# Kernel optimization log

Hardware: AMD Instinct MI355X
Metric: run time of the kernel (lower is better)

The kernel has to match this reference:

```python
import jax, jax.numpy as jnp
import numpy as np

N, E, F, H, C = 100000, 3200000, 128, 256, 47
EPS = 1e-5


def setup_inputs() -> dict:
    key = jax.random.key(0)
    ks = jax.random.split(key, 12)
    x = jax.random.normal(ks[0], (N, F), dtype=jnp.float32)
    edge_index = jax.random.randint(ks[1], (2, E), 0, N, dtype=jnp.int64)
    relations = jax.random.randint(ks[2], (E,), 0, 4, dtype=jnp.int64)
    def lin(k, fan_in, fan_out):
        return jax.random.normal(k, (fan_in, fan_out), dtype=jnp.float32) / np.sqrt(fan_in)
    W0 = lin(ks[3], F, H); b0 = jnp.zeros((H,), jnp.float32)
    W1 = lin(ks[4], H, H); b1 = jnp.zeros((H,), jnp.float32)
    W2 = lin(ks[5], H, C); b2 = jnp.zeros((C,), jnp.float32)
    g0 = jnp.ones((H,), jnp.float32); be0 = jnp.zeros((H,), jnp.float32)
    g1 = jnp.ones((H,), jnp.float32); be1 = jnp.zeros((H,), jnp.float32)
    return {"x": x, "edge_index": edge_index, "relations": relations,
            "W0": W0, "b0": b0, "g0": g0, "be0": be0,
            "W1": W1, "b1": b1, "g1": g1, "be1": be1,
            "W2": W2, "b2": b2}


def _gcn_conv(x, W, b, src, dst, n_nodes):
    # GCNConv: linear transform, add self-loops, symmetric degree normalization,
    # gather-scale-scatter aggregation, bias add.
    h = x @ W  # [N, out]
    self_loop = jnp.arange(n_nodes, dtype=src.dtype)
    s = jnp.concatenate([src, self_loop])
    d = jnp.concatenate([dst, self_loop])
    deg = jax.ops.segment_sum(jnp.ones(d.shape[0], h.dtype), d, num_segments=n_nodes)
    dinv = jnp.where(deg > 0, jax.lax.rsqrt(deg), 0.0)
    coef = dinv[s] * dinv[d]  # [E+N]
    out = jax.ops.segment_sum(h[s] * coef[:, None], d, num_segments=n_nodes)
    return out + b


def _batch_norm(x, gamma, beta):
    mean = jnp.mean(x, axis=0)
    var = jnp.var(x, axis=0)
    return (x - mean) * jax.lax.rsqrt(var + EPS) * gamma + beta


def reference(x, edge_index, relations, W0, b0, g0, be0, W1, b1, g1, be1, W2, b2):
    src, dst = edge_index[0], edge_index[1]
    n = x.shape[0]
    h = _gcn_conv(x, W0, b0, src, dst, n)
    h = jax.nn.relu(_batch_norm(h, g0, be0))  # dropout is identity in eval
    h = _gcn_conv(h, W1, b1, src, dst, n)
    h = jax.nn.relu(_batch_norm(h, g1, be1))
    h = _gcn_conv(h, W2, b2, src, dst, n)
    return jax.nn.log_softmax(h, axis=-1)
```

## Files before the change

### kernel.cpp

```cpp
#include <hip/hip_runtime.h>
#include <hip/hip_fp8.h>
#include <math.h>

#define NN 100000
#define NE 3200000
#define FIN 128
#define HD 256
#define CO 47
#define NBKT 196
#define G 1024
#define CHUNK 3125

typedef _Float16 h2 __attribute__((ext_vector_type(2)));
typedef _Float16 h4 __attribute__((ext_vector_type(4)));
typedef _Float16 h8 __attribute__((ext_vector_type(8)));
typedef float f32x2 __attribute__((ext_vector_type(2)));
typedef float f32x4 __attribute__((ext_vector_type(4)));
typedef unsigned int u32x2 __attribute__((ext_vector_type(2)));
typedef unsigned int u32x4 __attribute__((ext_vector_type(4)));


__global__ __launch_bounds__(256) void hist_kernel(const int* __restrict__ dst,
                                                   int* __restrict__ hist) {
    __shared__ int h[NBKT];
    int tid = threadIdx.x;
    for (int i = tid; i < NBKT; i += 256) h[i] = 0;
    __syncthreads();
    int base = blockIdx.x * CHUNK;
    for (int i = tid; i < CHUNK; i += 256)
        atomicAdd(&h[dst[base + i] >> 9], 1);
    __syncthreads();
    for (int i = tid; i < NBKT; i += 256) hist[i * G + blockIdx.x] = h[i];
}

__global__ __launch_bounds__(256) void rowscan_kernel(int* __restrict__ hist,
                                                      int* __restrict__ btot) {
    __shared__ int sums[256];
    int b = blockIdx.x, t = threadIdx.x;
    int base = b * G + t * 4;
    int4 v = *(int4*)&hist[base];
    int i0 = v.x, i1 = i0 + v.y, i2 = i1 + v.z, i3 = i2 + v.w;
    sums[t] = i3;
    __syncthreads();
    #pragma unroll
    for (int off = 1; off < 256; off <<= 1) {
        int u = (t >= off) ? sums[t - off] : 0;
        __syncthreads();
        sums[t] += u;
        __syncthreads();
    }
    int excl = sums[t] - i3;
    hist[base] = excl;
    hist[base + 1] = excl + i0;
    hist[base + 2] = excl + i1;
    hist[base + 3] = excl + i2;
    if (t == 255) btot[b] = sums[255];
}

__global__ void totscan_kernel(const int* __restrict__ btot, int* __restrict__ bbase) {
    __shared__ int tmp[256];
    int t = threadIdx.x;
    int v = (t < NBKT) ? btot[t] : 0;
    tmp[t] = v;
    __syncthreads();
    #pragma unroll
    for (int off = 1; off < 256; off <<= 1) {
        int u = (t >= off) ? tmp[t - off] : 0;
        __syncthreads();
        tmp[t] += u;
        __syncthreads();
    }
    if (t < NBKT) bbase[t] = tmp[t] - v;
    if (t == NBKT - 1) bbase[NBKT] = tmp[t];
}

__global__ __launch_bounds__(256) void scatter_kernel(const int* __restrict__ src,
                                                      const int* __restrict__ dst,
                                                      const int* __restrict__ hscan,
                                                      const int* __restrict__ bbase,
                                                      int* __restrict__ epk) {
    __shared__ int cur[NBKT];
    int tid = threadIdx.x;
    for (int i = tid; i < NBKT; i += 256)
        cur[i] = hscan[i * G + blockIdx.x] + bbase[i];
    __syncthreads();
    int base = blockIdx.x * CHUNK;
    for (int i = tid; i < CHUNK; i += 256) {
        int e = base + i;
        int d = dst[e];
        int slot = atomicAdd(&cur[d >> 9], 1);
        epk[slot] = ((d & 511) << 17) | src[e];
    }
}

__global__ __launch_bounds__(256) void bucket_fill_kernel(
    const int* __restrict__ bbase, const int* __restrict__ epk,
    int* __restrict__ csr, int* __restrict__ offs, float* __restrict__ dinv)
{
    __shared__ int deg[512], cur[512], a0[512], a1[512];
    int tid = threadIdx.x, b = blockIdx.x;
    int ebeg = bbase[b], eend = bbase[b + 1];
    deg[tid] = 0; deg[tid + 256] = 0;
    __syncthreads();
    for (int e = ebeg + tid; e < eend; e += 256)
        atomicAdd(&deg[((unsigned)epk[e]) >> 17], 1);
    __syncthreads();
    a0[tid] = deg[tid]; a0[tid + 256] = deg[tid + 256];
    __syncthreads();
    int* pin = a0; int* pout = a1;
    for (int off = 1; off < 512; off <<= 1) {
        #pragma unroll
        for (int q = 0; q < 2; ++q) {
            int p = tid + q * 256;
            pout[p] = pin[p] + ((p >= off) ? pin[p - off] : 0);
        }
        __syncthreads();
        int* t = pin; pin = pout; pout = t;
    }
    #pragma unroll
    for (int q = 0; q < 2; ++q) {
        int i = tid + q * 256;
        int excl = pin[i] - deg[i];
        cur[i] = excl;
        int node = b * 512 + i;
        if (node < NN) {
            offs[node] = ebeg + excl;
            dinv[node] = rsqrtf((float)deg[i] + 1.0f);
        }
    }
    if (b == 0 && tid == 0) offs[NN] = NE;
    __syncthreads();
    for (int e = ebeg + tid; e < eend; e += 256) {
        int pk = epk[e];
        int p = atomicAdd(&cur[((unsigned)pk) >> 17], 1);
        csr[ebeg + p] = pk & 0x1FFFF;
    }
}


template<int K>
__global__ void wtrans_kernel(const float* __restrict__ W, _Float16* __restrict__ Wt,
                              int N, int NP) {
    int i = blockIdx.x * 256 + threadIdx.x;
    if (i >= NP * K) return;
    int n = i / K, k = i % K;
    float v = (n < N) ? W[(size_t)k * N + n] : 0.0f;
    Wt[i] = (_Float16)v;
}


__global__ void conv_x_kernel(const float* __restrict__ x, const float* __restrict__ dinv,
                              unsigned* __restrict__ xq) {
    int i = blockIdx.x * 256 + threadIdx.x;
    if (i >= NN * FIN / 4) return;
    int r = i >> 5;
    float4 v = ((const float4*)x)[i];
    float dv = dinv[r];
    int u = __builtin_amdgcn_cvt_pk_fp8_f32(v.x * dv, v.y * dv, 0, false);
    u = __builtin_amdgcn_cvt_pk_fp8_f32(v.z * dv, v.w * dv, u, true);
    xq[i] = (unsigned)u;
}


__global__ __launch_bounds__(256) void agg128_kernel(
    const unsigned short* __restrict__ xq, const int* __restrict__ offs,
    const int* __restrict__ csr, const float* __restrict__ dinv,
    _Float16* __restrict__ out)
{
    int lane = threadIdx.x & 63;
    int v = blockIdx.x * 4 + (threadIdx.x >> 6);
    unsigned sv = xq[(size_t)v * 64 + lane];
    f32x2 acc = __builtin_amdgcn_cvt_pk_f32_fp8((int)sv, false);
    int b = offs[v], e = offs[v + 1], j = b;
    int s[8];
    if (j + 8 <= e) {
        #pragma unroll
        for (int q = 0; q < 8; ++q) s[q] = csr[j + q];
    }
    for (; j + 8 <= e; ) {
        int nj = j + 8;
        int ns[8];
        if (nj + 8 <= e) {
            #pragma unroll
            for (int q = 0; q < 8; ++q) ns[q] = csr[nj + q];
        }
        #pragma unroll
        for (int q = 0; q < 8; ++q) {
            unsigned t = xq[(size_t)s[q] * 64 + lane];
            acc += __builtin_amdgcn_cvt_pk_f32_fp8((int)t, false);
        }
        #pragma unroll
        for (int q = 0; q < 8; ++q) s[q] = ns[q];
        j = nj;
    }
    for (; j < e; ++j) {
        unsigned t = xq[(size_t)csr[j] * 64 + lane];
        acc += __builtin_amdgcn_cvt_pk_f32_fp8((int)t, false);
    }
    float dv = dinv[v];
    h2 o; o[0] = (_Float16)(acc[0] * dv); o[1] = (_Float16)(acc[1] * dv);
    ((h2*)out)[(size_t)v * 64 + lane] = o;
}

__global__ __launch_bounds__(256) void agg256_kernel(
    const unsigned* __restrict__ t1q, const int* __restrict__ offs,
    const int* __restrict__ csr, const float* __restrict__ dinv,
    unsigned* __restrict__ out)
{
    int lane = threadIdx.x & 63;
    int v = blockIdx.x * 4 + (threadIdx.x >> 6);
    unsigned sv = t1q[(size_t)v * 64 + lane];
    f32x2 acc01 = __builtin_amdgcn_cvt_pk_f32_fp8((int)sv, false);
    f32x2 acc23 = __builtin_amdgcn_cvt_pk_f32_fp8((int)sv, true);
    int b = offs[v], e = offs[v + 1], j = b;
    int s[8];
    if (j + 8 <= e) {
        #pragma unroll
        for (int q = 0; q < 8; ++q) s[q] = csr[j + q];
    }
    for (; j + 8 <= e; ) {
        int nj = j + 8;
        int ns[8];
        if (nj + 8 <= e) {
            #pragma unroll
            for (int q = 0; q < 8; ++q) ns[q] = csr[nj + q];
        }
        #pragma unroll
        for (int q = 0; q < 8; ++q) {
            unsigned t = t1q[(size_t)s[q] * 64 + lane];
            acc01 += __builtin_amdgcn_cvt_pk_f32_fp8((int)t, false);
            acc23 += __builtin_amdgcn_cvt_pk_f32_fp8((int)t, true);
        }
        #pragma unroll
        for (int q = 0; q < 8; ++q) s[q] = ns[q];
        j = nj;
    }
    for (; j < e; ++j) {
        unsigned t = t1q[(size_t)csr[j] * 64 + lane];
        acc01 += __builtin_amdgcn_cvt_pk_f32_fp8((int)t, false);
        acc23 += __builtin_amdgcn_cvt_pk_f32_fp8((int)t, true);
    }
    float dv = dinv[v];
    int pk = __builtin_amdgcn_cvt_pk_fp8_f32(acc01[0] * dv, acc01[1] * dv, 0, false);
    pk = __builtin_amdgcn_cvt_pk_fp8_f32(acc23[0] * dv, acc23[1] * dv, pk, true);
    out[(size_t)v * 64 + lane] = (unsigned)pk;
}

__global__ __launch_bounds__(256) void agg47_lsm_kernel(
    const unsigned* __restrict__ t2q, const int* __restrict__ offs,
    const int* __restrict__ csr, const float* __restrict__ dinv,
    const float* __restrict__ bias, float* __restrict__ out)
{
    int lane = threadIdx.x & 63;
    int v = blockIdx.x * 4 + (threadIdx.x >> 6);
    bool act = lane < 16;
    f32x2 a01 = {0.f, 0.f}, a23 = {0.f, 0.f};
    if (act) {
        unsigned u = t2q[(size_t)v * 16 + lane];
        a01 = __builtin_amdgcn_cvt_pk_f32_fp8((int)u, false);
        a23 = __builtin_amdgcn_cvt_pk_f32_fp8((int)u, true);
    }
    int b = offs[v], e = offs[v + 1], j = b;
    int s[8];
    if (j + 8 <= e) {
        #pragma unroll
        for (int q = 0; q < 8; ++q) s[q] = csr[j + q];
    }
    for (; j + 8 <= e; ) {
        int nj = j + 8;
        int ns[8];
        if (nj + 8 <= e) {
            #pragma unroll
            for (int q = 0; q < 8; ++q) ns[q] = csr[nj + q];
        }
        if (act) {
            #pragma unroll
            for (int q = 0; q < 8; ++q) {
                unsigned t = t2q[(size_t)s[q] * 16 + lane];
                a01 += __builtin_amdgcn_cvt_pk_f32_fp8((int)t, false);
                a23 += __builtin_amdgcn_cvt_pk_f32_fp8((int)t, true);
            }
        }
        #pragma unroll
        for (int q = 0; q < 8; ++q) s[q] = ns[q];
        j = nj;
    }
    for (; j < e; ++j) {
        if (act) {
            unsigned t = t2q[(size_t)csr[j] * 16 + lane];
            a01 += __builtin_amdgcn_cvt_pk_f32_fp8((int)t, false);
            a23 += __builtin_amdgcn_cvt_pk_f32_fp8((int)t, true);
        }
    }
    float dv = dinv[v];
    float vals[4] = {a01[0], a01[1], a23[0], a23[1]};
    float vv[4];
    #pragma unroll
    for (int k = 0; k < 4; ++k) {
        int c = 4 * lane + k;
        vv[k] = (act && c < CO) ? fmaf(vals[k], dv, bias[c]) : -1e30f;
    }
    float m = fmaxf(fmaxf(vv[0], vv[1]), fmaxf(vv[2], vv[3]));
    #pragma unroll
    for (int o = 8; o > 0; o >>= 1) m = fmaxf(m, __shfl_xor(m, o, 64));
    float sum = 0.f;
    #pragma unroll
    for (int k = 0; k < 4; ++k) sum += (vv[k] > -1e29f) ? expf(vv[k] - m) : 0.f;
    #pragma unroll
    for (int o = 8; o > 0; o >>= 1) sum += __shfl_xor(sum, o, 64);
    float lse = m + logf(sum);
    if (act) {
        #pragma unroll
        for (int k = 0; k < 4; ++k) {
            int c = 4 * lane + k;
            if (c < CO) out[(size_t)v * CO + c] = vv[k] - lse;
        }
    }
}


#define LDS_PAD 8

template<int K, bool XFORM, bool EPI_DINV, bool OUT8, bool BNSTAT>
__global__ __launch_bounds__(256) void mfma_gemm_big(
    const _Float16* __restrict__ A, int lda,
    const _Float16* __restrict__ Wt,
    const float* __restrict__ ss, const float* __restrict__ dinv,
    void* __restrict__ outp, int ldo, float* __restrict__ part8)
{
    __shared__ __align__(16) _Float16 As[128][64 + LDS_PAD];
    __shared__ __align__(16) _Float16 Bs[128][64 + LDS_PAD];
    __shared__ float SS[2 * K];
    __shared__ float cstat[256];
    const int row0 = (blockIdx.x >> 1) * 128;
    const int col0 = (blockIdx.x & 1) * 128;
    const int tid = threadIdx.x;
    if (XFORM) {
        for (int i = tid; i < 2 * K; i += 256) SS[i] = ss[i];
    }
    if (BNSTAT) cstat[tid] = 0.f;
    const int lane = tid & 63;
    const int wv = tid >> 6;
    const int wr = wv >> 1, wc = wv & 1;
    const int fr = lane & 15;
    const int kb = (lane >> 4) * 8;

    f32x4 acc[4][4];
    #pragma unroll
    for (int m = 0; m < 4; ++m)
        #pragma unroll
        for (int n = 0; n < 4; ++n)
            acc[m][n] = (f32x4){0.f, 0.f, 0.f, 0.f};

    if (XFORM || BNSTAT) __syncthreads();

    for (int k0 = 0; k0 < K; k0 += 64) {
        #pragma unroll
        for (int p = 0; p < 4; ++p) {
            int c = p * 256 + tid;
            int m = c >> 3, kk = (c & 7) * 8;
            int r = row0 + m;
            h8 av = {};
            if (r < NN) av = *(const h8*)&A[(size_t)r * lda + k0 + kk];
            if (XFORM) {
                #pragma unroll
                for (int j = 0; j < 8; ++j) {
                    float a = (float)av[j];
                    a = fmaxf(fmaf(a, SS[k0 + kk + j], SS[K + k0 + kk + j]), 0.0f);
                    av[j] = (_Float16)a;
                }
            }
            *(h8*)&As[m][kk] = av;
        }
        #pragma unroll
        for (int p = 0; p < 4; ++p) {
            int c = p * 256 + tid;
            int n = c >> 3, kk = (c & 7) * 8;
            h8 bv = *(const h8*)&Wt[(size_t)(col0 + n) * K + k0 + kk];
            *(h8*)&Bs[n][kk] = bv;
        }
        __syncthreads();
        #pragma unroll
        for (int ks = 0; ks < 2; ++ks) {
            h8 a[4], b[4];
            #pragma unroll
            for (int m = 0; m < 4; ++m)
                a[m] = *(const h8*)&As[wr * 64 + m * 16 + fr][ks * 32 + kb];
            #pragma unroll
            for (int n = 0; n < 4; ++n)
                b[n] = *(const h8*)&Bs[wc * 64 + n * 16 + fr][ks * 32 + kb];
            #pragma unroll
            for (int m = 0; m < 4; ++m)
                #pragma unroll
                for (int n = 0; n < 4; ++n)
                    acc[m][n] = __builtin_amdgcn_mfma_f32_16x16x32_f16(a[m], b[n], acc[m][n], 0, 0, 0);
        }
        __syncthreads();
    }

    const int fq = lane >> 4;
    if (OUT8) {
        unsigned char* stg = (unsigned char*)&As[0][0];
        #pragma unroll
        for (int m = 0; m < 4; ++m) {
            #pragma unroll
            for (int j = 0; j < 4; ++j) {
                int rr = wr * 64 + m * 16 + fq * 4 + j;
                int r = row0 + rr;
                float dv = (EPI_DINV && r < NN) ? dinv[r] : 1.0f;
                #pragma unroll
                for (int n = 0; n < 4; n += 2) {
                    int cc0 = wc * 64 + n * 16 + fr;
                    float v0 = acc[m][n][j] * dv;
                    float v1 = acc[m][n + 1][j] * dv;
                    int pk = __builtin_amdgcn_cvt_pk_fp8_f32(v0, v1, 0, false);
                    stg[rr * 128 + cc0] = (unsigned char)(pk & 0xFF);
                    stg[rr * 128 + cc0 + 16] = (unsigned char)((pk >> 8) & 0xFF);
                }
            }
        }
        __syncthreads();
        #pragma unroll
        for (int p = 0; p < 4; ++p) {
            int rr = p * 32 + (tid >> 3);
            int cc = (tid & 7) * 16;
            int r = row0 + rr;
            if (r < NN)
                *(u32x4*)&((unsigned char*)outp)[(size_t)r * ldo + col0 + cc] =
                    *(u32x4*)&stg[rr * 128 + cc];
        }
    } else {
        float ps[4] = {}, pq[4] = {};
        #pragma unroll
        for (int m = 0; m < 4; ++m) {
            #pragma unroll
            for (int j = 0; j < 4; ++j) {
                int r = row0 + wr * 64 + m * 16 + fq * 4 + j;
                if (r >= NN) continue;
                float dv = EPI_DINV ? dinv[r] : 1.0f;
                #pragma unroll
                for (int n = 0; n < 4; ++n) {
                    int c = col0 + wc * 64 + n * 16 + fr;
                    float val = acc[m][n][j] * dv;
                    ((_Float16*)outp)[(size_t)r * ldo + c] = (_Float16)val;
                    if (BNSTAT) { ps[n] += val; pq[n] += val * val; }
                }
            }
        }
        if (BNSTAT) {
            #pragma unroll
            for (int n = 0; n < 4; ++n) {
                int cc = wc * 64 + n * 16 + fr;
                atomicAdd(&cstat[cc], ps[n]);
                atomicAdd(&cstat[128 + cc], pq[n]);
            }
            __syncthreads();
            if (tid < 128) {
                int rep = (blockIdx.x & 7) * 512;
                atomicAdd(&part8[rep + col0 + tid], cstat[tid]);
                atomicAdd(&part8[rep + 256 + col0 + tid], cstat[128 + tid]);
            }
        }
    }
}


__global__ __launch_bounds__(256) void mfma_gemm2_kernel(
    const unsigned* __restrict__ Aq,
    const _Float16* __restrict__ Wt,
    const float* __restrict__ ss, const float* __restrict__ dinv,
    unsigned char* __restrict__ t2q)
{
    __shared__ __align__(16) _Float16 As[128][32 + LDS_PAD];
    __shared__ __align__(16) _Float16 Bs[64][32 + LDS_PAD];
    __shared__ float SS[2 * HD];
    const int row0 = blockIdx.x * 128;
    const int tid = threadIdx.x;
    for (int i = tid; i < 2 * HD; i += 256) SS[i] = ss[i];
    const int lane = tid & 63;
    const int wv = tid >> 6;
    const int wr = wv >> 1, wc = wv & 1;
    const int fr = lane & 15;
    const int kb = (lane >> 4) * 8;

    f32x4 acc[4][2];
    #pragma unroll
    for (int m = 0; m < 4; ++m)
        #pragma unroll
        for (int n = 0; n < 2; ++n)
            acc[m][n] = (f32x4){0.f, 0.f, 0.f, 0.f};

    __syncthreads();

    for (int k0 = 0; k0 < HD; k0 += 32) {
        #pragma unroll
        for (int p = 0; p < 2; ++p) {
            int idx = (p * 256 + tid) * 8;
            int m = idx >> 5, kk = idx & 31;
            int r = row0 + m;
            float vals[8] = {};
            if (r < NN) {
                u32x2 u = *(const u32x2*)&Aq[(size_t)r * 64 + ((k0 + kk) >> 2)];
                f32x2 p0 = __builtin_amdgcn_cvt_pk_f32_fp8((int)u[0], false);
                f32x2 p1 = __builtin_amdgcn_cvt_pk_f32_fp8((int)u[0], true);
                f32x2 p2 = __builtin_amdgcn_cvt_pk_f32_fp8((int)u[1], false);
                f32x2 p3 = __builtin_amdgcn_cvt_pk_f32_fp8((int)u[1], true);
                vals[0] = p0[0]; vals[1] = p0[1]; vals[2] = p1[0]; vals[3] = p1[1];
                vals[4] = p2[0]; vals[5] = p2[1]; vals[6] = p3[0]; vals[7] = p3[1];
            }
            h8 av;
            #pragma unroll
            for (int j = 0; j < 8; ++j) {
                float a = fmaxf(fmaf(vals[j], SS[k0 + kk + j], SS[HD + k0 + kk + j]), 0.0f);
                av[j] = (_Float16)a;
            }
            *(h8*)&As[m][kk] = av;
        }
        {
            int idx = tid * 8;
            int n = idx >> 5, kk = idx & 31;
            h8 bv = *(const h8*)&Wt[(size_t)n * HD + k0 + kk];
            *(h8*)&Bs[n][kk] = bv;
        }
        __syncthreads();
        h8 a[4], b[2];
        #pragma unroll
        for (int m = 0; m < 4; ++m)
            a[m] = *(const h8*)&As[wr * 64 + m * 16 + fr][kb];
        #pragma unroll
        for (int n = 0; n < 2; ++n)
            b[n] = *(const h8*)&Bs[wc * 32 + n * 16 + fr][kb];
        #pragma unroll
        for (int m = 0; m < 4; ++m)
            #pragma unroll
            for (int n = 0; n < 2; ++n)
                acc[m][n] = __builtin_amdgcn_mfma_f32_16x16x32_f16(a[m], b[n], acc[m][n], 0, 0, 0);
        __syncthreads();
    }

    const int fq = lane >> 4;
    unsigned char* stg = (unsigned char*)&As[0][0];
    #pragma unroll
    for (int m = 0; m < 4; ++m) {
        #pragma unroll
        for (int j = 0; j < 4; ++j) {
            int rr = wr * 64 + m * 16 + fq * 4 + j;
            int r = row0 + rr;
            float dv = (r < NN) ? dinv[r] : 1.0f;
            int cc0 = wc * 32 + fr;
            float v0 = acc[m][0][j] * dv;
            float v1 = acc[m][1][j] * dv;
            int pk = __builtin_amdgcn_cvt_pk_fp8_f32(v0, v1, 0, false);
            stg[rr * 64 + cc0] = (unsigned char)(pk & 0xFF);
            stg[rr * 64 + cc0 + 16] = (unsigned char)((pk >> 8) & 0xFF);
        }
    }
    __syncthreads();
    #pragma unroll
    for (int p = 0; p < 2; ++p) {
        int idx = p * 256 + tid;
        int rr = idx >> 2;
        int cc = (idx & 3) * 16;
        int r = row0 + rr;
        if (r < NN)
            *(u32x4*)&t2q[(size_t)r * 64 + cc] = *(u32x4*)&stg[rr * 64 + cc];
    }
}


__global__ void bn_finalize8_kernel(const float* __restrict__ part8,
                                    const float* __restrict__ g,
                                    const float* __restrict__ be,
                                    float* __restrict__ ss) {
    int t = threadIdx.x;
    float s1 = 0.f, s2 = 0.f;
    #pragma unroll
    for (int x = 0; x < 8; ++x) {
        s1 += part8[x * 512 + t];
        s2 += part8[x * 512 + 256 + t];
    }
    float mean = s1 * (1.0f / NN);
    float var = s2 * (1.0f / NN) - mean * mean;
    float sc = g[t] * rsqrtf(var + 1e-5f);
    ss[t] = sc;
    ss[HD + t] = be[t] - mean * sc;
}

__global__ __launch_bounds__(256) void bn_part8_kernel(const unsigned* __restrict__ h,
                                                       float* __restrict__ part) {
    int tid = threadIdx.x;
    int fg = tid & 63;
    int rg = tid >> 6;
    float s1[4] = {}, s2[4] = {};
    for (int r = blockIdx.x * 4 + rg; r < NN; r += 4096) {
        unsigned u = h[(size_t)r * 64 + fg];
        f32x2 a = __builtin_amdgcn_cvt_pk_f32_fp8((int)u, false);
        f32x2 b = __builtin_amdgcn_cvt_pk_f32_fp8((int)u, true);
        float f0 = a[0], f1 = a[1], f2 = b[0], f3 = b[1];
        s1[0] += f0; s2[0] += f0 * f0;
        s1[1] += f1; s2[1] += f1 * f1;
        s1[2] += f2; s2[2] += f2 * f2;
        s1[3] += f3; s2[3] += f3 * f3;
    }
    __shared__ float sm[256][8];
    #pragma unroll
    for (int j = 0; j < 4; ++j) { sm[tid][j] = s1[j]; sm[tid][4 + j] = s2[j]; }
    __syncthreads();
    if (tid < 64) {
        float o1[4] = {}, o2[4] = {};
        #pragma unroll
        for (int r = 0; r < 4; ++r)
            #pragma unroll
            for (int j = 0; j < 4; ++j) {
                o1[j] += sm[r * 64 + tid][j];
                o2[j] += sm[r * 64 + tid][4 + j];
            }
        #pragma unroll
        for (int j = 0; j < 4; ++j) {
            part[(size_t)blockIdx.x * 512 + tid * 4 + j] = o1[j];
            part[(size_t)blockIdx.x * 512 + 256 + tid * 4 + j] = o2[j];
        }
    }
}

__global__ __launch_bounds__(256) void bn_reduce_kernel(const float* __restrict__ part,
                                                        const float* __restrict__ g,
                                                        const float* __restrict__ be,
                                                        float* __restrict__ ss) {
    int f = blockIdx.x * 32 + (threadIdx.x & 31);
    int c = threadIdx.x >> 5;
    float s1 = 0.f, s2 = 0.f;
    for (int b = c; b < 1024; b += 8) {
        s1 += part[(size_t)b * 512 + f];
        s2 += part[(size_t)b * 512 + 256 + f];
    }
    __shared__ float m1[8][32], m2[8][32];
    m1[c][threadIdx.x & 31] = s1; m2[c][threadIdx.x & 31] = s2;
    __syncthreads();
    if (threadIdx.x < 32) {
        float t1 = 0.f, t2 = 0.f;
        #pragma unroll
        for (int q = 0; q < 8; ++q) { t1 += m1[q][threadIdx.x]; t2 += m2[q][threadIdx.x]; }
        float mean = t1 * (1.0f / NN);
        float var = t2 * (1.0f / NN) - mean * mean;
        float sc = g[f] * rsqrtf(var + 1e-5f);
        ss[f] = sc;
        ss[HD + f] = be[f] - mean * sc;
    }
}


extern "C" void kernel_launch(void* const* d_in, const int* in_sizes, int n_in,
                              void* d_out, int out_size, void* d_ws, size_t ws_size,
                              hipStream_t stream) {
    const float* x   = (const float*)d_in[0];
    const int*   ei  = (const int*)d_in[1];
    const float* W0  = (const float*)d_in[3];
    const float* g0  = (const float*)d_in[5];
    const float* be0 = (const float*)d_in[6];
    const float* W1  = (const float*)d_in[7];
    const float* g1  = (const float*)d_in[9];
    const float* be1 = (const float*)d_in[10];
    const float* W2  = (const float*)d_in[11];
    const float* b2  = (const float*)d_in[12];
    float* out = (float*)d_out;

    const int* src = ei;
    const int* dst = ei + NE;

    const size_t S = 51200000;
    char* ws = (char*)d_ws;
    unsigned*       xq  = (unsigned*)ws;
    unsigned*       t1q = (unsigned*)ws;
    unsigned char*  t2q = (unsigned char*)ws;
    _Float16*       a0  = (_Float16*)(ws + 25600000);
    _Float16*       S2  = (_Float16*)(ws + S);
    unsigned*       h1q = (unsigned*)(ws + S);
    char* base2 = ws + 2 * S;
    int*   csr  = (int*)  (base2);
    int*   offs = (int*)  (base2 + 12800000);
    float* dinv = (float*)(base2 + 13200064);
    float* ssb  = (float*)(base2 + 13602112);
    int*   btot = (int*)  (base2 + 13604160);
    int*   bbase= (int*)  (base2 + 13605184);
    _Float16* wt0 = (_Float16*)(base2 + 13608320);
    _Float16* wt1 = (_Float16*)(base2 + 13673856);
    _Float16* wt2 = (_Float16*)(base2 + 13804928);
    int*   hist = (int*)  (base2 + 13837696);
    int*   epk  = (int*)  (base2 + 14640576);
    float* part = (float*)(base2 + 27440576);
    float* part8= (float*)(base2 + 29537728);

    hist_kernel<<<G, 256, 0, stream>>>(dst, hist);
    rowscan_kernel<<<NBKT, 256, 0, stream>>>(hist, btot);
    totscan_kernel<<<1, 256, 0, stream>>>(btot, bbase);
    scatter_kernel<<<G, 256, 0, stream>>>(src, dst, hist, bbase, epk);
    bucket_fill_kernel<<<NBKT, 256, 0, stream>>>(bbase, epk, csr, offs, dinv);

    wtrans_kernel<FIN><<<(256 * FIN + 255) / 256, 256, 0, stream>>>(W0, wt0, HD, HD);
    wtrans_kernel<HD><<<(256 * HD + 255) / 256, 256, 0, stream>>>(W1, wt1, HD, HD);
    wtrans_kernel<HD><<<(64 * HD + 255) / 256, 256, 0, stream>>>(W2, wt2, CO, 64);

    const int MB = (NN + 127) / 128;

    hipMemsetAsync(part8, 0, 8 * 512 * sizeof(float), stream);
    conv_x_kernel<<<(NN * FIN / 4 + 255) / 256, 256, 0, stream>>>(x, dinv, xq);
    agg128_kernel<<<NN / 4, 256, 0, stream>>>((const unsigned short*)xq, offs, csr, dinv, a0);
    mfma_gemm_big<FIN, false, false, false, true><<<MB * 2, 256, 0, stream>>>(
        a0, FIN, wt0, nullptr, dinv, S2, HD, part8);
    bn_finalize8_kernel<<<1, HD, 0, stream>>>(part8, g0, be0, ssb);

    mfma_gemm_big<HD, true, true, true, false><<<MB * 2, 256, 0, stream>>>(
        S2, HD, wt1, ssb, dinv, t1q, HD, nullptr);
    agg256_kernel<<<NN / 4, 256, 0, stream>>>(t1q, offs, csr, dinv, h1q);

    bn_part8_kernel<<<1024, 256, 0, stream>>>(h1q, part);
    bn_reduce_kernel<<<8, 256, 0, stream>>>(part, g1, be1, ssb);

    mfma_gemm2_kernel<<<MB, 256, 0, stream>>>(h1q, wt2, ssb, dinv, t2q);
    agg47_lsm_kernel<<<NN / 4, 256, 0, stream>>>((const unsigned*)t2q, offs, csr, dinv, b2, out);
}
```

Measured before the change: 554.8 us.

## Split wavefront into edge sub-groups in narrow aggregation kernels and fuse weight transposes

The 128-wide and 47-wide aggregation kernels now split each 64-lane wavefront into 2 or 4 lane groups. Each group gathers a different interleaved subset of a node's neighbors using 4-byte loads, and the partial sums are combined with cross-lane shuffles at the end. In the 47-class kernel this puts the previously idle 48 lanes to work, and in the 128 kernel each gather uses wider loads. The three weight-transpose launches are merged into one kernel to cut launch overhead. The cost is extra shuffle reductions and a longer tail loop for low-degree nodes.

```diff
diff --git a/kernel.cpp b/kernel.cpp
--- a/kernel.cpp
+++ b/kernel.cpp
@@ -138,14 +138,25 @@
 }
 
 
-template<int K>
-__global__ void wtrans_kernel(const float* __restrict__ W, _Float16* __restrict__ Wt,
-                              int N, int NP) {
+__global__ void wtrans_all_kernel(const float* __restrict__ W0,
+                                  const float* __restrict__ W1,
+                                  const float* __restrict__ W2,
+                                  _Float16* __restrict__ wt0,
+                                  _Float16* __restrict__ wt1,
+                                  _Float16* __restrict__ wt2) {
     int i = blockIdx.x * 256 + threadIdx.x;
-    if (i >= NP * K) return;
-    int n = i / K, k = i % K;
-    float v = (n < N) ? W[(size_t)k * N + n] : 0.0f;
-    Wt[i] = (_Float16)v;
+    if (i < 256 * 128) {
+        int n = i >> 7, k = i & 127;
+        wt0[i] = (_Float16)W0[k * 256 + n];
+    } else if (i < 256 * 128 + 256 * 256) {
+        int t = i - 256 * 128;
+        int n = t >> 8, k = t & 255;
+        wt1[t] = (_Float16)W1[k * 256 + n];
+    } else if (i < 256 * 128 + 256 * 256 + 64 * 256) {
+        int t = i - 256 * 128 - 256 * 256;
+        int n = t >> 8, k = t & 255;
+        wt2[t] = (_Float16)((n < CO) ? W2[k * CO + n] : 0.0f);
+    }
 }
 
 
@@ -163,43 +174,61 @@
 
 
 __global__ __launch_bounds__(256) void agg128_kernel(
-    const unsigned short* __restrict__ xq, const int* __restrict__ offs,
+    const unsigned* __restrict__ xq, const int* __restrict__ offs,
     const int* __restrict__ csr, const float* __restrict__ dinv,
     _Float16* __restrict__ out)
 {
     int lane = threadIdx.x & 63;
+    int grp = lane >> 5;
+    int gl = lane & 31;
     int v = blockIdx.x * 4 + (threadIdx.x >> 6);
-    unsigned sv = xq[(size_t)v * 64 + lane];
-    f32x2 acc = __builtin_amdgcn_cvt_pk_f32_fp8((int)sv, false);
-    int b = offs[v], e = offs[v + 1], j = b;
+    f32x2 a01 = {0.f, 0.f}, a23 = {0.f, 0.f};
+    if (grp == 0) {
+        unsigned sv = xq[(size_t)v * 32 + gl];
+        a01 += __builtin_amdgcn_cvt_pk_f32_fp8((int)sv, false);
+        a23 += __builtin_amdgcn_cvt_pk_f32_fp8((int)sv, true);
+    }
+    int b = offs[v], e = offs[v + 1];
+    int j = b + grp;
     int s[8];
-    if (j + 8 <= e) {
-        #pragma unroll
-        for (int q = 0; q < 8; ++q) s[q] = csr[j + q];
-    }
-    for (; j + 8 <= e; ) {
-        int nj = j + 8;
+    bool have = (j + 14 < e);
+    if (have) {
+        #pragma unroll
+        for (int q = 0; q < 8; ++q) s[q] = csr[j + 2 * q];
+    }
+    while (have) {
+        int nj = j + 16;
+        bool nhave = (nj + 14 < e);
         int ns[8];
-        if (nj + 8 <= e) {
-            #pragma unroll
-            for (int q = 0; q < 8; ++q) ns[q] = csr[nj + q];
+        if (nhave) {
+            #pragma unroll
+            for (int q = 0; q < 8; ++q) ns[q] = csr[nj + 2 * q];
         }
         #pragma unroll
         for (int q = 0; q < 8; ++q) {
-            unsigned t = xq[(size_t)s[q] * 64 + lane];
-            acc += __builtin_amdgcn_cvt_pk_f32_fp8((int)t, false);
+            unsigned t = xq[(size_t)s[q] * 32 + gl];
+            a01 += __builtin_amdgcn_cvt_pk_f32_fp8((int)t, false);
+            a23 += __builtin_amdgcn_cvt_pk_f32_fp8((int)t, true);
         }
         #pragma unroll
         for (int q = 0; q < 8; ++q) s[q] = ns[q];
-        j = nj;
-    }
-    for (; j < e; ++j) {
-        unsigned t = xq[(size_t)csr[j] * 64 + lane];
-        acc += __builtin_amdgcn_cvt_pk_f32_fp8((int)t, false);
-    }
-    float dv = dinv[v];
-    h2 o; o[0] = (_Float16)(acc[0] * dv); o[1] = (_Float16)(acc[1] * dv);
-    ((h2*)out)[(size_t)v * 64 + lane] = o;
+        j = nj; have = nhave;
+    }
+    for (; j < e; j += 2) {
+        unsigned t = xq[(size_t)csr[j] * 32 + gl];
+        a01 += __builtin_amdgcn_cvt_pk_f32_fp8((int)t, false);
+        a23 += __builtin_amdgcn_cvt_pk_f32_fp8((int)t, true);
+    }
+    a01[0] += __shfl_xor(a01[0], 32, 64);
+    a01[1] += __shfl_xor(a01[1], 32, 64);
+    a23[0] += __shfl_xor(a23[0], 32, 64);
+    a23[1] += __shfl_xor(a23[1], 32, 64);
+    if (grp == 0) {
+        float dv = dinv[v];
+        h4 o; o[0] = (_Float16)(a01[0] * dv); o[1] = (_Float16)(a01[1] * dv);
+        o[2] = (_Float16)(a23[0] * dv); o[3] = (_Float16)(a23[1] * dv);
+        ((h4*)out)[(size_t)v * 32 + gl] = o;
+    }
 }
 
 __global__ __launch_bounds__(256) void agg256_kernel(
@@ -252,53 +281,60 @@
     const float* __restrict__ bias, float* __restrict__ out)
 {
     int lane = threadIdx.x & 63;
+    int grp = lane >> 4;
+    int gl = lane & 15;
     int v = blockIdx.x * 4 + (threadIdx.x >> 6);
-    bool act = lane < 16;
     f32x2 a01 = {0.f, 0.f}, a23 = {0.f, 0.f};
-    if (act) {
-        unsigned u = t2q[(size_t)v * 16 + lane];
-        a01 = __builtin_amdgcn_cvt_pk_f32_fp8((int)u, false);
-        a23 = __builtin_amdgcn_cvt_pk_f32_fp8((int)u, true);
-    }
-    int b = offs[v], e = offs[v + 1], j = b;
+    if (grp == 0) {
+        unsigned u = t2q[(size_t)v * 16 + gl];
+        a01 += __builtin_amdgcn_cvt_pk_f32_fp8((int)u, false);
+        a23 += __builtin_amdgcn_cvt_pk_f32_fp8((int)u, true);
+    }
+    int b = offs[v], e = offs[v + 1];
+    int j = b + grp;
     int s[8];
-    if (j + 8 <= e) {
-        #pragma unroll
-        for (int q = 0; q < 8; ++q) s[q] = csr[j + q];
-    }
-    for (; j + 8 <= e; ) {
-        int nj = j + 8;
+    bool have = (j + 28 < e);
+    if (have) {
+        #pragma unroll
+        for (int q = 0; q < 8; ++q) s[q] = csr[j + 4 * q];
+    }
+    while (have) {
+        int nj = j + 32;
+        bool nhave = (nj + 28 < e);
         int ns[8];
-        if (nj + 8 <= e) {
-            #pragma unroll
-            for (int q = 0; q < 8; ++q) ns[q] = csr[nj + q];
-        }
-        if (act) {
-            #pragma unroll
-            for (int q = 0; q < 8; ++q) {
-                unsigned t = t2q[(size_t)s[q] * 16 + lane];
-                a01 += __builtin_amdgcn_cvt_pk_f32_fp8((int)t, false);
-                a23 += __builtin_amdgcn_cvt_pk_f32_fp8((int)t, true);
-            }
-        }
-        #pragma unroll
-        for (int q = 0; q < 8; ++q) s[q] = ns[q];
-        j = nj;
-    }
-    for (; j < e; ++j) {
-        if (act) {
-            unsigned t = t2q[(size_t)csr[j] * 16 + lane];
+        if (nhave) {
+            #pragma unroll
+            for (int q = 0; q < 8; ++q) ns[q] = csr[nj + 4 * q];
+        }
+        #pragma unroll
+        for (int q = 0; q < 8; ++q) {
+            unsigned t = t2q[(size_t)s[q] * 16 + gl];
             a01 += __builtin_amdgcn_cvt_pk_f32_fp8((int)t, false);
             a23 += __builtin_amdgcn_cvt_pk_f32_fp8((int)t, true);
         }
+        #pragma unroll
+        for (int q = 0; q < 8; ++q) s[q] = ns[q];
+        j = nj; have = nhave;
+    }
+    for (; j < e; j += 4) {
+        unsigned t = t2q[(size_t)csr[j] * 16 + gl];
+        a01 += __builtin_amdgcn_cvt_pk_f32_fp8((int)t, false);
+        a23 += __builtin_amdgcn_cvt_pk_f32_fp8((int)t, true);
+    }
+    #pragma unroll
+    for (int o = 16; o <= 32; o <<= 1) {
+        a01[0] += __shfl_xor(a01[0], o, 64);
+        a01[1] += __shfl_xor(a01[1], o, 64);
+        a23[0] += __shfl_xor(a23[0], o, 64);
+        a23[1] += __shfl_xor(a23[1], o, 64);
     }
     float dv = dinv[v];
     float vals[4] = {a01[0], a01[1], a23[0], a23[1]};
     float vv[4];
     #pragma unroll
     for (int k = 0; k < 4; ++k) {
-        int c = 4 * lane + k;
-        vv[k] = (act && c < CO) ? fmaf(vals[k], dv, bias[c]) : -1e30f;
+        int c = 4 * gl + k;
+        vv[k] = (c < CO) ? fmaf(vals[k], dv, bias[c]) : -1e30f;
     }
     float m = fmaxf(fmaxf(vv[0], vv[1]), fmaxf(vv[2], vv[3]));
     #pragma unroll
@@ -309,10 +345,10 @@
     #pragma unroll
     for (int o = 8; o > 0; o >>= 1) sum += __shfl_xor(sum, o, 64);
     float lse = m + logf(sum);
-    if (act) {
+    if (grp == 0) {
         #pragma unroll
         for (int k = 0; k < 4; ++k) {
-            int c = 4 * lane + k;
+            int c = 4 * gl + k;
             if (c < CO) out[(size_t)v * CO + c] = vv[k] - lse;
         }
     }
@@ -697,15 +733,13 @@
     scatter_kernel<<<G, 256, 0, stream>>>(src, dst, hist, bbase, epk);
     bucket_fill_kernel<<<NBKT, 256, 0, stream>>>(bbase, epk, csr, offs, dinv);
 
-    wtrans_kernel<FIN><<<(256 * FIN + 255) / 256, 256, 0, stream>>>(W0, wt0, HD, HD);
-    wtrans_kernel<HD><<<(256 * HD + 255) / 256, 256, 0, stream>>>(W1, wt1, HD, HD);
-    wtrans_kernel<HD><<<(64 * HD + 255) / 256, 256, 0, stream>>>(W2, wt2, CO, 64);
+    wtrans_all_kernel<<<448, 256, 0, stream>>>(W0, W1, W2, wt0, wt1, wt2);
 
     const int MB = (NN + 127) / 128;
 
     hipMemsetAsync(part8, 0, 8 * 512 * sizeof(float), stream);
     conv_x_kernel<<<(NN * FIN / 4 + 255) / 256, 256, 0, stream>>>(x, dinv, xq);
-    agg128_kernel<<<NN / 4, 256, 0, stream>>>((const unsigned short*)xq, offs, csr, dinv, a0);
+    agg128_kernel<<<NN / 4, 256, 0, stream>>>(xq, offs, csr, dinv, a0);
     mfma_gemm_big<FIN, false, false, false, true><<<MB * 2, 256, 0, stream>>>(
         a0, FIN, wt0, nullptr, dinv, S2, HD, part8);
     bn_finalize8_kernel<<<1, HD, 0, stream>>>(part8, g0, be0, ssb);
```

New measurement: 545.8 us (median of 2 runs). No clear change (-1.6%).
